# Optimization experiments

Measured on AMD Instinct MI355X. Metric: run time of the kernel, lower is better.

The kernel has to match this reference:

```python
import jax, jax.numpy as jnp
import numpy as np

N = 50000          # nodes
E = 800000         # edges (first N are self-loops -> no zero in-degree)
IN = 128           # in_feats
OUT = 64           # out_feats per head
MAP = 128          # map_feats
H = 4              # num_heads


def setup_inputs() -> dict:
    key = jax.random.key(0)
    ks = jax.random.split(key, 10)
    x = jax.random.normal(ks[0], (N, IN), jnp.float32)
    src = jnp.concatenate([jnp.arange(N), jax.random.randint(ks[1], (E - N,), 0, N)]).astype(jnp.int32)
    dst = jnp.concatenate([jnp.arange(N), jax.random.randint(ks[2], (E - N,), 0, N)]).astype(jnp.int32)
    weight = jax.random.uniform(ks[3], (E,), jnp.float32)
    s = lambda k, shape, fan: jax.random.normal(k, shape, jnp.float32) / np.sqrt(fan).astype(np.float32)
    fc_w = s(ks[4], (H * OUT, IN), IN)
    attn_l = s(ks[5], (H, OUT), OUT)
    attn_r = s(ks[6], (H, OUT), OUT)
    gate_m_w = s(ks[7], (MAP, IN), IN)
    gate_m_b = jnp.zeros((MAP,), jnp.float32)
    gate_fn_w = s(ks[8], (H, 2 * IN + MAP), 2 * IN + MAP)
    gate_fn_b = jnp.zeros((H,), jnp.float32)
    merger_w = s(ks[9], (OUT, IN + OUT), IN + OUT)
    merger_b = jnp.zeros((OUT,), jnp.float32)
    return dict(x=x, src=src, dst=dst, weight=weight, fc_w=fc_w, attn_l=attn_l,
                attn_r=attn_r, gate_m_w=gate_m_w, gate_m_b=gate_m_b,
                gate_fn_w=gate_fn_w, gate_fn_b=gate_fn_b,
                merger_w=merger_w, merger_b=merger_b)


def reference(x, src, dst, weight, fc_w, attn_l, attn_r, gate_m_w, gate_m_b,
              gate_fn_w, gate_fn_b, merger_w, merger_b):
    seg_sum = lambda v: jax.ops.segment_sum(v, dst, num_segments=N)
    seg_max = lambda v: jax.ops.segment_max(v, dst, num_segments=N)
    deg = seg_sum(jnp.ones((E,), x.dtype))                      # [N] in-degree

    # ---- gate path: mailbox max of gate_m(z) and mean of z over in-neighbors ----
    mz = x @ gate_m_w.T + gate_m_b                              # [N, MAP]
    max_z = seg_max(mz[src])                                    # [N, MAP]
    max_z = jnp.where(jnp.isfinite(max_z), max_z, 0.0)          # guard empty segments
    mean_z = seg_sum(x[src]) / jnp.maximum(deg, 1.0)[:, None]   # [N, IN]
    gate = jax.nn.sigmoid(
        jnp.concatenate([x, max_z, mean_z], axis=1) @ gate_fn_w.T + gate_fn_b)  # [N, H]

    # ---- weighted GAT path ----
    feat = (x @ fc_w.T).reshape(N, H, OUT)                      # [N, H, OUT]
    el = jnp.einsum('nhd,hd->nh', feat, attn_l)                 # [N, H]
    er = jnp.einsum('nhd,hd->nh', feat, attn_r)
    e = jax.nn.leaky_relu(el[src] + er[dst], negative_slope=0.2)  # [E, H]
    emax = seg_max(e)
    emax = jnp.where(jnp.isfinite(emax), emax, 0.0)
    ex = jnp.exp(e - emax[dst])                                 # [E, H]
    a = ex / seg_sum(ex)[dst]                                   # edge softmax per (dst, head)
    a = a * weight[:, None]                                     # per-edge weight scaling
    rst = seg_sum(feat[src] * a[:, :, None])                    # [N, H, OUT]

    # ---- gated merge ----
    gated = (gate[:, :, None] * rst).mean(axis=1)               # [N, OUT]
    return jnp.concatenate([x, gated], axis=1) @ merger_w.T + merger_b
```

## Files before the change

kernel.cpp:

```cpp
#include <hip/hip_runtime.h>
#include <math.h>

#define NN 50000
#define EE 800000
#define GEMM_BLKS 391
#define SCAT_BLKS 512
#define MAXDEG 64
#define RSH 9
#define LOG2E 1.44269504088896340736f

typedef short s8v __attribute__((ext_vector_type(8)));
typedef float f4v __attribute__((ext_vector_type(4)));
typedef float f2v __attribute__((ext_vector_type(2)));

__device__ inline unsigned short f2bf(float f) {
    unsigned u = __float_as_uint(f);
    unsigned r = (u + 0x7FFFu + ((u >> 16) & 1u)) >> 16;
    return (unsigned short)r;
}

__global__ __launch_bounds__(256) void fused_prep(const float* __restrict__ x,
                                                  const float* __restrict__ fc_w,
                                                  const float* __restrict__ gate_m_w,
                                                  const float* __restrict__ merger_w,
                                                  const float* __restrict__ gate_fn_w,
                                                  unsigned short* __restrict__ xb,
                                                  unsigned short* __restrict__ wb,
                                                  unsigned short* __restrict__ wmb,
                                                  char* __restrict__ rec) {
    int tid = threadIdx.x;
    int lane = tid & 63, wv = tid >> 6;
    int l5 = lane & 31;
    int n = blockIdx.x * 8 + wv * 2 + (lane >> 5);

    if (n < NN) {
        float4 xv = *(const float4*)(x + (size_t)n * 128 + 4 * l5);
        ushort4 o;
        o.x = f2bf(xv.x); o.y = f2bf(xv.y); o.z = f2bf(xv.z); o.w = f2bf(xv.w);
        *(ushort4*)&xb[(size_t)n * 128 + 4 * l5] = o;

        float p1[4], p3[4];
        #pragma unroll
        for (int h = 0; h < 4; ++h) {
            float4 g0 = *(const float4*)(gate_fn_w + h * 384 + 4 * l5);
            float4 g2 = *(const float4*)(gate_fn_w + h * 384 + 256 + 4 * l5);
            p1[h] = g0.x * xv.x + g0.y * xv.y + g0.z * xv.z + g0.w * xv.w;
            p3[h] = g2.x * xv.x + g2.y * xv.y + g2.z * xv.z + g2.w * xv.w;
        }
        #pragma unroll
        for (int o2 = 1; o2 < 32; o2 <<= 1) {
            #pragma unroll
            for (int h = 0; h < 4; ++h) {
                p1[h] += __shfl_xor(p1[h], o2, 64);
                p3[h] += __shfl_xor(p3[h], o2, 64);
            }
        }
        if (l5 == 0) {
            *(float4*)(rec + ((size_t)n << RSH) + 16) = make_float4(p3[0], p3[1], p3[2], p3[3]);
            *(float4*)(rec + ((size_t)n << RSH) + 48) = make_float4(p1[0], p1[1], p1[2], p1[3]);
        }
    }

    int gtid = blockIdx.x * 256 + tid;
    int total = gridDim.x * 256;
    for (int i = gtid; i < 384 * 128; i += total)
        wb[i] = f2bf(i < 256 * 128 ? fc_w[i] : gate_m_w[i - 256 * 128]);
    for (int i = gtid; i < 64 * 192; i += total)
        wmb[i] = f2bf(merger_w[i]);
}

__global__ __launch_bounds__(256, 3) void gemm_scatter(const unsigned short* __restrict__ xb,
                                                       const unsigned short* __restrict__ wb,
                                                       const float* __restrict__ gate_m_b,
                                                       const float* __restrict__ attn_l,
                                                       const float* __restrict__ attn_r,
                                                       char* __restrict__ rec,
                                                       const int* __restrict__ src,
                                                       const int* __restrict__ dst,
                                                       const float* __restrict__ weight,
                                                       int* __restrict__ cnt,
                                                       unsigned* __restrict__ sw_pad) {
    int blk = blockIdx.x;
    if (blk >= 3 * GEMM_BLKS) {
        int bid = blk - 3 * GEMM_BLKS;
        int stride4 = SCAT_BLKS * 256 * 4;
        for (int i = (bid * 256 + threadIdx.x) * 4; i < EE; i += stride4) {
            int4 d4 = *(const int4*)(dst + i);
            int4 s4 = *(const int4*)(src + i);
            float4 w4 = *(const float4*)(weight + i);
            int p0 = atomicAdd(&cnt[d4.x], 1);
            int p1 = atomicAdd(&cnt[d4.y], 1);
            int p2 = atomicAdd(&cnt[d4.z], 1);
            int p3 = atomicAdd(&cnt[d4.w], 1);
            if (p0 < MAXDEG) sw_pad[(d4.x << 6) + p0] = ((unsigned)f2bf(w4.x) << 16) | (unsigned)s4.x;
            if (p1 < MAXDEG) sw_pad[(d4.y << 6) + p1] = ((unsigned)f2bf(w4.y) << 16) | (unsigned)s4.y;
            if (p2 < MAXDEG) sw_pad[(d4.z << 6) + p2] = ((unsigned)f2bf(w4.z) << 16) | (unsigned)s4.z;
            if (p3 < MAXDEG) sw_pad[(d4.w << 6) + p3] = ((unsigned)f2bf(w4.w) << 16) | (unsigned)s4.w;
        }
        return;
    }
    int tid = threadIdx.x;
    int lane = tid & 63, w = tid >> 6;
    int wr = w >> 1, wc = w & 1;
    int lrow = lane & 15, lhi = lane >> 4;
    int row0 = (blk % GEMM_BLKS) * 128;
    int jc = blk / GEMM_BLKS;
    int colbase = jc * 128 + wc * 64;

    int xrow[4];
    const unsigned short* bp[4];
    #pragma unroll
    for (int xrf = 0; xrf < 4; ++xrf) {
        int r = row0 + wr * 64 + xrf * 16 + lrow;
        xrow[xrf] = r;
        int rc = (r < NN) ? r : (NN - 1);
        bp[xrf] = xb + (size_t)rc * 128 + lhi * 8;
    }
    const unsigned short* ap[4];
    #pragma unroll
    for (int ocf = 0; ocf < 4; ++ocf)
        ap[ocf] = wb + (size_t)(colbase + ocf * 16 + lrow) * 128 + lhi * 8;

    f4v acc[4][4] = {};
    #pragma unroll
    for (int kk = 0; kk < 4; ++kk) {
        s8v a[4], b[4];
        #pragma unroll
        for (int ocf = 0; ocf < 4; ++ocf) a[ocf] = *(const s8v*)(ap[ocf] + kk * 32);
        #pragma unroll
        for (int xrf = 0; xrf < 4; ++xrf) b[xrf] = *(const s8v*)(bp[xrf] + kk * 32);
        #pragma unroll
        for (int ocf = 0; ocf < 4; ++ocf)
            #pragma unroll
            for (int xrf = 0; xrf < 4; ++xrf)
                acc[ocf][xrf] = __builtin_amdgcn_mfma_f32_16x16x32_bf16(a[ocf], b[xrf], acc[ocf][xrf], 0, 0, 0);
    }

    #pragma unroll
    for (int ocf = 0; ocf < 4; ++ocf) {
        int gcol0 = colbase + ocf * 16 + lhi * 4;
        float4 bias = make_float4(0.f, 0.f, 0.f, 0.f);
        if (jc == 2) bias = *(const float4*)&gate_m_b[gcol0 - 256];
        #pragma unroll
        for (int xrf = 0; xrf < 4; ++xrf) {
            if (xrow[xrf] < NN) {
                int r = __builtin_amdgcn_cvt_pk_fp8_f32(acc[ocf][xrf][0] + bias.x,
                                                        acc[ocf][xrf][1] + bias.y, 0, false);
                r = __builtin_amdgcn_cvt_pk_fp8_f32(acc[ocf][xrf][2] + bias.z,
                                                    acc[ocf][xrf][3] + bias.w, r, true);
                *(int*)(rec + ((size_t)xrow[xrf] << RSH) + 64 + gcol0) = r;
            }
        }
    }

    if (jc < 2) {
        int head = jc * 2 + wc;
        float4 al[4], ar[4];
        #pragma unroll
        for (int ocf = 0; ocf < 4; ++ocf) {
            al[ocf] = *(const float4*)&attn_l[head * 64 + ocf * 16 + lhi * 4];
            ar[ocf] = *(const float4*)&attn_r[head * 64 + ocf * 16 + lhi * 4];
        }
        #pragma unroll
        for (int xrf = 0; xrf < 4; ++xrf) {
            float tl = 0.f, tr = 0.f;
            #pragma unroll
            for (int ocf = 0; ocf < 4; ++ocf) {
                tl += acc[ocf][xrf][0] * al[ocf].x + acc[ocf][xrf][1] * al[ocf].y
                    + acc[ocf][xrf][2] * al[ocf].z + acc[ocf][xrf][3] * al[ocf].w;
                tr += acc[ocf][xrf][0] * ar[ocf].x + acc[ocf][xrf][1] * ar[ocf].y
                    + acc[ocf][xrf][2] * ar[ocf].z + acc[ocf][xrf][3] * ar[ocf].w;
            }
            tl += __shfl_xor(tl, 16, 64); tl += __shfl_xor(tl, 32, 64);
            tr += __shfl_xor(tr, 16, 64); tr += __shfl_xor(tr, 32, 64);
            if (lhi == 0 && xrow[xrf] < NN) {
                *(float*)(rec + ((size_t)xrow[xrf] << RSH) + head * 4) = tl * LOG2E;
                *(float*)(rec + ((size_t)xrow[xrf] << RSH) + 32 + head * 4) = tr * LOG2E;
            }
        }
    }
}

__global__ __launch_bounds__(256, 8) void node_kernel(const char* __restrict__ rec,
                                                      const int* __restrict__ cnt,
                                                      const unsigned* __restrict__ sw_pad,
                                                      const float* __restrict__ gate_fn_w,
                                                      const float* __restrict__ gate_fn_b,
                                                      unsigned short* __restrict__ gb) {
    int lane = threadIdx.x & 63, wv = threadIdx.x >> 6;
    int n = blockIdx.x * 4 + wv;
    if (n >= NN) return;
    int deg = cnt[n];
    if (deg > MAXDEG) deg = MAXDEG;
    const unsigned* swr = sw_pad + ((size_t)n << 6);
    int half = lane >> 5;
    int l5 = lane & 31;
    int h = l5 >> 3;
    unsigned oE = (unsigned)(h << 2);
    unsigned oF = 64u + (unsigned)(l5 << 3);
    unsigned oM = 320u + (unsigned)(l5 << 2);

    float ern   = *(const float*)(rec + ((unsigned)n << RSH) + 32 + (h << 2));
    float d1own = *(const float*)(rec + ((unsigned)n << RSH) + 48 + (h << 2));

    float mzv0 = -INFINITY, mzv1 = -INFINITY, mzv2 = -INFINITY, mzv3 = -INFINITY;
    float sd = 0.f, se = 0.f;
    float ac0 = 0, ac1 = 0, ac2 = 0, ac3 = 0, ac4 = 0, ac5 = 0, ac6 = 0, ac7 = 0;

    int idx = 0;
    for (; idx + 4 <= deg; idx += 4) {
        uint4 sv = *(const uint4*)(swr + idx);
        unsigned eA = half ? sv.y : sv.x;
        unsigned eB = half ? sv.w : sv.z;
        unsigned bA = (eA & 0xFFFFu) << RSH;
        unsigned bB = (eB & 0xFFFFu) << RSH;
        float wA = __uint_as_float(eA & 0xFFFF0000u);
        float wB = __uint_as_float(eB & 0xFFFF0000u);

        float elA = *(const float*)(rec + (bA + oE));
        float dxA = *(const float*)(rec + (bA + oE) + 16);
        uint2 fA  = *(const uint2*)(rec + (bA + oF));
        unsigned mA = *(const unsigned*)(rec + (bA + oM));
        float elB = *(const float*)(rec + (bB + oE));
        float dxB = *(const float*)(rec + (bB + oE) + 16);
        uint2 fB  = *(const uint2*)(rec + (bB + oF));
        unsigned mB = *(const unsigned*)(rec + (bB + oM));

        float s, ex, aw;
        f2v q;
        s = elA + ern; s = fmaxf(s, 0.2f * s);
        ex = __builtin_amdgcn_exp2f(s);
        se += ex; aw = ex * wA;
        q = __builtin_amdgcn_cvt_pk_f32_fp8(fA.x, false); ac0 += aw * q[0]; ac1 += aw * q[1];
        q = __builtin_amdgcn_cvt_pk_f32_fp8(fA.x, true);  ac2 += aw * q[0]; ac3 += aw * q[1];
        q = __builtin_amdgcn_cvt_pk_f32_fp8(fA.y, false); ac4 += aw * q[0]; ac5 += aw * q[1];
        q = __builtin_amdgcn_cvt_pk_f32_fp8(fA.y, true);  ac6 += aw * q[0]; ac7 += aw * q[1];
        q = __builtin_amdgcn_cvt_pk_f32_fp8(mA, false); mzv0 = fmaxf(mzv0, q[0]); mzv1 = fmaxf(mzv1, q[1]);
        q = __builtin_amdgcn_cvt_pk_f32_fp8(mA, true);  mzv2 = fmaxf(mzv2, q[0]); mzv3 = fmaxf(mzv3, q[1]);
        sd += dxA;

        s = elB + ern; s = fmaxf(s, 0.2f * s);
        ex = __builtin_amdgcn_exp2f(s);
        se += ex; aw = ex * wB;
        q = __builtin_amdgcn_cvt_pk_f32_fp8(fB.x, false); ac0 += aw * q[0]; ac1 += aw * q[1];
        q = __builtin_amdgcn_cvt_pk_f32_fp8(fB.x, true);  ac2 += aw * q[0]; ac3 += aw * q[1];
        q = __builtin_amdgcn_cvt_pk_f32_fp8(fB.y, false); ac4 += aw * q[0]; ac5 += aw * q[1];
        q = __builtin_amdgcn_cvt_pk_f32_fp8(fB.y, true);  ac6 += aw * q[0]; ac7 += aw * q[1];
        q = __builtin_amdgcn_cvt_pk_f32_fp8(mB, false); mzv0 = fmaxf(mzv0, q[0]); mzv1 = fmaxf(mzv1, q[1]);
        q = __builtin_amdgcn_cvt_pk_f32_fp8(mB, true);  mzv2 = fmaxf(mzv2, q[0]); mzv3 = fmaxf(mzv3, q[1]);
        sd += dxB;
    }
    if (idx + 2 <= deg) {
        uint2 sv = *(const uint2*)(swr + idx);
        unsigned eA = half ? sv.y : sv.x;
        unsigned bA = (eA & 0xFFFFu) << RSH;
        float wA = __uint_as_float(eA & 0xFFFF0000u);
        float elA = *(const float*)(rec + (bA + oE));
        float dxA = *(const float*)(rec + (bA + oE) + 16);
        uint2 fA  = *(const uint2*)(rec + (bA + oF));
        unsigned mA = *(const unsigned*)(rec + (bA + oM));
        float s = elA + ern; s = fmaxf(s, 0.2f * s);
        float ex = __builtin_amdgcn_exp2f(s);
        se += ex; float aw = ex * wA;
        f2v q;
        q = __builtin_amdgcn_cvt_pk_f32_fp8(fA.x, false); ac0 += aw * q[0]; ac1 += aw * q[1];
        q = __builtin_amdgcn_cvt_pk_f32_fp8(fA.x, true);  ac2 += aw * q[0]; ac3 += aw * q[1];
        q = __builtin_amdgcn_cvt_pk_f32_fp8(fA.y, false); ac4 += aw * q[0]; ac5 += aw * q[1];
        q = __builtin_amdgcn_cvt_pk_f32_fp8(fA.y, true);  ac6 += aw * q[0]; ac7 += aw * q[1];
        q = __builtin_amdgcn_cvt_pk_f32_fp8(mA, false); mzv0 = fmaxf(mzv0, q[0]); mzv1 = fmaxf(mzv1, q[1]);
        q = __builtin_amdgcn_cvt_pk_f32_fp8(mA, true);  mzv2 = fmaxf(mzv2, q[0]); mzv3 = fmaxf(mzv3, q[1]);
        sd += dxA;
        idx += 2;
    }
    if (idx < deg) {
        unsigned e = swr[idx];
        unsigned b = (e & 0xFFFFu) << RSH;
        float elv = *(const float*)(rec + (b + oE));
        float dxv = *(const float*)(rec + (b + oE) + 16);
        uint2 fw  = *(const uint2*)(rec + (b + oF));
        unsigned mw = *(const unsigned*)(rec + (b + oM));
        float s = elv + ern; s = fmaxf(s, 0.2f * s);
        float ex = (half == 0) ? __builtin_amdgcn_exp2f(s) : 0.f;
        se += ex; float aw = ex * __uint_as_float(e & 0xFFFF0000u);
        f2v q;
        q = __builtin_amdgcn_cvt_pk_f32_fp8(fw.x, false); ac0 += aw * q[0]; ac1 += aw * q[1];
        q = __builtin_amdgcn_cvt_pk_f32_fp8(fw.x, true);  ac2 += aw * q[0]; ac3 += aw * q[1];
        q = __builtin_amdgcn_cvt_pk_f32_fp8(fw.y, false); ac4 += aw * q[0]; ac5 += aw * q[1];
        q = __builtin_amdgcn_cvt_pk_f32_fp8(fw.y, true);  ac6 += aw * q[0]; ac7 += aw * q[1];
        if (half == 0) {
            q = __builtin_amdgcn_cvt_pk_f32_fp8(mw, false); mzv0 = fmaxf(mzv0, q[0]); mzv1 = fmaxf(mzv1, q[1]);
            q = __builtin_amdgcn_cvt_pk_f32_fp8(mw, true);  mzv2 = fmaxf(mzv2, q[0]); mzv3 = fmaxf(mzv3, q[1]);
            sd += dxv;
        }
    }

    se += __shfl_xor(se, 32, 64);
    sd += __shfl_xor(sd, 32, 64);
    mzv0 = fmaxf(mzv0, __shfl_xor(mzv0, 32, 64));
    mzv1 = fmaxf(mzv1, __shfl_xor(mzv1, 32, 64));
    mzv2 = fmaxf(mzv2, __shfl_xor(mzv2, 32, 64));
    mzv3 = fmaxf(mzv3, __shfl_xor(mzv3, 32, 64));
    ac0 += __shfl_xor(ac0, 32, 64); ac1 += __shfl_xor(ac1, 32, 64);
    ac2 += __shfl_xor(ac2, 32, 64); ac3 += __shfl_xor(ac3, 32, 64);
    ac4 += __shfl_xor(ac4, 32, 64); ac5 += __shfl_xor(ac5, 32, 64);
    ac6 += __shfl_xor(ac6, 32, 64); ac7 += __shfl_xor(ac7, 32, 64);

    if (deg == 0) { mzv0 = mzv1 = mzv2 = mzv3 = 0.f; }
    float invd = 1.0f / fmaxf((float)deg, 1.0f);

    float p[4];
    #pragma unroll
    for (int hh = 0; hh < 4; ++hh) {
        float4 g1 = *(const float4*)(gate_fn_w + hh * 384 + 128 + 4 * l5);
        p[hh] = g1.x * mzv0 + g1.y * mzv1 + g1.z * mzv2 + g1.w * mzv3;
    }
    #pragma unroll
    for (int o = 1; o < 32; o <<= 1) {
        #pragma unroll
        for (int hh = 0; hh < 4; ++hh) p[hh] += __shfl_xor(p[hh], o, 64);
    }
    bool sA = (lane & 8) != 0, sB = (lane & 16) != 0;
    float p01 = sA ? p[1] : p[0];
    float p23 = sA ? p[3] : p[2];
    float pown = sB ? p23 : p01;
    float bown = gate_fn_b[h];

    float gown = 1.0f / (1.0f + __expf(-(d1own + sd * invd + pown + bown)));
    float scale = 0.25f * gown / fmaxf(se, 1e-30f);

    ac0 *= scale; ac1 *= scale; ac2 *= scale; ac3 *= scale;
    ac4 *= scale; ac5 *= scale; ac6 *= scale; ac7 *= scale;
    ac0 += __shfl_xor(ac0, 8, 64); ac1 += __shfl_xor(ac1, 8, 64);
    ac2 += __shfl_xor(ac2, 8, 64); ac3 += __shfl_xor(ac3, 8, 64);
    ac4 += __shfl_xor(ac4, 8, 64); ac5 += __shfl_xor(ac5, 8, 64);
    ac6 += __shfl_xor(ac6, 8, 64); ac7 += __shfl_xor(ac7, 8, 64);
    ac0 += __shfl_xor(ac0, 16, 64); ac1 += __shfl_xor(ac1, 16, 64);
    ac2 += __shfl_xor(ac2, 16, 64); ac3 += __shfl_xor(ac3, 16, 64);
    ac4 += __shfl_xor(ac4, 16, 64); ac5 += __shfl_xor(ac5, 16, 64);
    ac6 += __shfl_xor(ac6, 16, 64); ac7 += __shfl_xor(ac7, 16, 64);

    if (lane < 8) {
        union { unsigned short u[8]; s8v v; } o;
        o.u[0] = f2bf(ac0); o.u[1] = f2bf(ac1); o.u[2] = f2bf(ac2); o.u[3] = f2bf(ac3);
        o.u[4] = f2bf(ac4); o.u[5] = f2bf(ac5); o.u[6] = f2bf(ac6); o.u[7] = f2bf(ac7);
        *(s8v*)&gb[(size_t)n * 64 + lane * 8] = o.v;
    }
}

__global__ __launch_bounds__(256) void merge_mfma(const unsigned short* __restrict__ xb,
                                                  const unsigned short* __restrict__ gb,
                                                  const unsigned short* __restrict__ wmb,
                                                  const float* __restrict__ merger_b,
                                                  float* __restrict__ out) {
    __shared__ unsigned short la[128 * 200];
    int tid = threadIdx.x;
    int row0 = blockIdx.x * 128;
    for (int c = tid; c < 128 * 24; c += 256) {
        int r = c / 24, seg = c % 24;
        int gr = row0 + r; if (gr >= NN) gr = NN - 1;
        s8v v = (seg < 16) ? *(const s8v*)&xb[(size_t)gr * 128 + seg * 8]
                           : *(const s8v*)&gb[(size_t)gr * 64 + (seg - 16) * 8];
        *(s8v*)&la[r * 200 + seg * 8] = v;
    }
    __syncthreads();

    int lane = tid & 63, w = tid >> 6;
    int lrow = lane & 15, lhi = lane >> 4;
    f4v acc[2][4] = {};
    const unsigned short* pa = &la[(w * 32 + lrow) * 200 + lhi * 8];
    #pragma unroll
    for (int kk = 0; kk < 6; ++kk) {
        s8v a0 = *(const s8v*)(pa + kk * 32);
        s8v a1 = *(const s8v*)(pa + 16 * 200 + kk * 32);
        #pragma unroll
        for (int ni = 0; ni < 4; ++ni) {
            s8v b = *(const s8v*)&wmb[(size_t)(ni * 16 + lrow) * 192 + kk * 32 + lhi * 8];
            acc[0][ni] = __builtin_amdgcn_mfma_f32_16x16x32_bf16(a0, b, acc[0][ni], 0, 0, 0);
            acc[1][ni] = __builtin_amdgcn_mfma_f32_16x16x32_bf16(a1, b, acc[1][ni], 0, 0, 0);
        }
    }
    #pragma unroll
    for (int ni = 0; ni < 4; ++ni) {
        int gcol = ni * 16 + lrow;
        float bias = merger_b[gcol];
        #pragma unroll
        for (int mi = 0; mi < 2; ++mi) {
            #pragma unroll
            for (int rg = 0; rg < 4; ++rg) {
                int grow = row0 + w * 32 + mi * 16 + lhi * 4 + rg;
                if (grow < NN) out[(size_t)grow * 64 + gcol] = acc[mi][ni][rg] + bias;
            }
        }
    }
}

extern "C" void kernel_launch(void* const* d_in, const int* in_sizes, int n_in,
                              void* d_out, int out_size, void* d_ws, size_t ws_size,
                              hipStream_t stream) {
    const float* x         = (const float*)d_in[0];
    const int*   src       = (const int*)d_in[1];
    const int*   dst       = (const int*)d_in[2];
    const float* weight    = (const float*)d_in[3];
    const float* fc_w      = (const float*)d_in[4];
    const float* attn_l    = (const float*)d_in[5];
    const float* attn_r    = (const float*)d_in[6];
    const float* gate_m_w  = (const float*)d_in[7];
    const float* gate_m_b  = (const float*)d_in[8];
    const float* gate_fn_w = (const float*)d_in[9];
    const float* gate_fn_b = (const float*)d_in[10];
    const float* merger_w  = (const float*)d_in[11];
    const float* merger_b  = (const float*)d_in[12];
    float* out = (float*)d_out;

    char* p = (char*)d_ws;
    auto alloc = [&](size_t bytes) {
        char* r = p;
        p += (bytes + 511) & ~(size_t)511;
        return r;
    };
    char* rec           = alloc((size_t)NN * 512);
    int*   cnt          = (int*)alloc((size_t)NN * 4);
    unsigned* sw_pad    = (unsigned*)alloc((size_t)NN * MAXDEG * 4);
    unsigned short* xb  = (unsigned short*)alloc((size_t)NN * 128 * 2);
    unsigned short* wb  = (unsigned short*)alloc((size_t)384 * 128 * 2);
    unsigned short* wmb = (unsigned short*)alloc((size_t)64 * 192 * 2);
    unsigned short* gbuf= (unsigned short*)alloc((size_t)NN * 64 * 2);

    (void)hipMemsetAsync(cnt, 0, (size_t)NN * 4, stream);
    fused_prep<<<(NN + 7) / 8, 256, 0, stream>>>(x, fc_w, gate_m_w, merger_w, gate_fn_w,
                                                 xb, wb, wmb, rec);
    gemm_scatter<<<3 * GEMM_BLKS + SCAT_BLKS, 256, 0, stream>>>(xb, wb, gate_m_b, attn_l, attn_r,
                                                                rec, src, dst, weight, cnt,
                                                                sw_pad);
    node_kernel<<<NN / 4, 256, 0, stream>>>(rec, cnt, sw_pad,
                                            gate_fn_w, gate_fn_b, gbuf);
    merge_mfma<<<(NN + 127) / 128, 256, 0, stream>>>(xb, gbuf, wmb, merger_b, out);
}
```

Before: 172.2 us.

## Partition edge scatter by destination range across block groups, schedule scatter first

```diff
diff --git a/kernel.cpp b/kernel.cpp
--- a/kernel.cpp
+++ b/kernel.cpp
@@ -4,7 +4,8 @@
 #define NN 50000
 #define EE 800000
 #define GEMM_BLKS 391
-#define SCAT_BLKS 512
+#define SCAT_BLKS 1024
+#define RANGE 6250
 #define MAXDEG 64
 #define RSH 9
 #define LOG2E 1.44269504088896340736f
@@ -81,24 +82,37 @@
                                                        int* __restrict__ cnt,
                                                        unsigned* __restrict__ sw_pad) {
     int blk = blockIdx.x;
-    if (blk >= 3 * GEMM_BLKS) {
-        int bid = blk - 3 * GEMM_BLKS;
-        int stride4 = SCAT_BLKS * 256 * 4;
-        for (int i = (bid * 256 + threadIdx.x) * 4; i < EE; i += stride4) {
+    if (blk < SCAT_BLKS) {
+        int lo = (blk & 7) * RANGE;
+        int hi = lo + RANGE;
+        int gid = (blk >> 3) * 256 + threadIdx.x;
+        int gstride4 = (SCAT_BLKS >> 3) * 256 * 4;
+        for (int i = gid * 4; i < EE; i += gstride4) {
             int4 d4 = *(const int4*)(dst + i);
-            int4 s4 = *(const int4*)(src + i);
-            float4 w4 = *(const float4*)(weight + i);
-            int p0 = atomicAdd(&cnt[d4.x], 1);
-            int p1 = atomicAdd(&cnt[d4.y], 1);
-            int p2 = atomicAdd(&cnt[d4.z], 1);
-            int p3 = atomicAdd(&cnt[d4.w], 1);
-            if (p0 < MAXDEG) sw_pad[(d4.x << 6) + p0] = ((unsigned)f2bf(w4.x) << 16) | (unsigned)s4.x;
-            if (p1 < MAXDEG) sw_pad[(d4.y << 6) + p1] = ((unsigned)f2bf(w4.y) << 16) | (unsigned)s4.y;
-            if (p2 < MAXDEG) sw_pad[(d4.z << 6) + p2] = ((unsigned)f2bf(w4.z) << 16) | (unsigned)s4.z;
-            if (p3 < MAXDEG) sw_pad[(d4.w << 6) + p3] = ((unsigned)f2bf(w4.w) << 16) | (unsigned)s4.w;
+            if (d4.x >= lo && d4.x < hi) {
+                int pos = atomicAdd(&cnt[d4.x], 1);
+                if (pos < MAXDEG)
+                    sw_pad[(d4.x << 6) + pos] = ((unsigned)f2bf(weight[i]) << 16) | (unsigned)src[i];
+            }
+            if (d4.y >= lo && d4.y < hi) {
+                int pos = atomicAdd(&cnt[d4.y], 1);
+                if (pos < MAXDEG)
+                    sw_pad[(d4.y << 6) + pos] = ((unsigned)f2bf(weight[i + 1]) << 16) | (unsigned)src[i + 1];
+            }
+            if (d4.z >= lo && d4.z < hi) {
+                int pos = atomicAdd(&cnt[d4.z], 1);
+                if (pos < MAXDEG)
+                    sw_pad[(d4.z << 6) + pos] = ((unsigned)f2bf(weight[i + 2]) << 16) | (unsigned)src[i + 2];
+            }
+            if (d4.w >= lo && d4.w < hi) {
+                int pos = atomicAdd(&cnt[d4.w], 1);
+                if (pos < MAXDEG)
+                    sw_pad[(d4.w << 6) + pos] = ((unsigned)f2bf(weight[i + 3]) << 16) | (unsigned)src[i + 3];
+            }
         }
         return;
     }
+    blk -= SCAT_BLKS;
     int tid = threadIdx.x;
     int lane = tid & 63, w = tid >> 6;
     int wr = w >> 1, wc = w & 1;
@@ -429,7 +443,7 @@
     (void)hipMemsetAsync(cnt, 0, (size_t)NN * 4, stream);
     fused_prep<<<(NN + 7) / 8, 256, 0, stream>>>(x, fc_w, gate_m_w, merger_w, gate_fn_w,
                                                  xb, wb, wmb, rec);
-    gemm_scatter<<<3 * GEMM_BLKS + SCAT_BLKS, 256, 0, stream>>>(xb, wb, gate_m_b, attn_l, attn_r,
+    gemm_scatter<<<SCAT_BLKS + 3 * GEMM_BLKS, 256, 0, stream>>>(xb, wb, gate_m_b, attn_l, attn_r,
                                                                 rec, src, dst, weight, cnt,
                                                                 sw_pad);
     node_kernel<<<NN / 4, 256, 0, stream>>>(rec, cnt, sw_pad,
```

Measured after the change: 166.6 us (median of 2 runs). -3.2%, faster.
